# Kernel optimization log

Measured on AMD Instinct MI355X. Metric: run time of the kernel, lower is better.

Reference implementation:

```python
import jax, jax.numpy as jnp
import numpy as np

N = 100000
E = 3200000
IN_CH = 512
H1 = 16


def setup_inputs() -> dict:
    key = jax.random.key(0)
    ks = jax.random.split(key, 9)
    x = jax.random.normal(ks[0], (N, IN_CH), dtype=jnp.float32)
    edge_index = jax.random.randint(ks[1], (2, E), 0, N, dtype=jnp.int64)
    # GCNConv params: weight [in, out], bias [out]
    def glorot(k, fan_in, fan_out):
        lim = (6.0 / (fan_in + fan_out)) ** 0.5
        return jax.random.uniform(k, (fan_in, fan_out), jnp.float32, -lim, lim)
    W1 = glorot(ks[2], IN_CH, H1)
    b1 = jnp.zeros((H1,), jnp.float32)
    W2 = glorot(ks[3], H1, H1)
    b2 = jnp.zeros((H1,), jnp.float32)
    W3 = glorot(ks[4], H1, 1)
    b3 = jnp.zeros((1,), jnp.float32)
    return {"x": x, "edge_index": edge_index, "W1": W1, "b1": b1,
            "W2": W2, "b2": b2, "W3": W3, "b3": b3}


def _gcn_conv(x, W, b, src, dst, deg_isqrt):
    # GCNConv: h = X W; out = D^-1/2 (A + I) D^-1/2 h + b
    h = x @ W  # [N, out]
    norm = deg_isqrt[src] * deg_isqrt[dst]  # [E]
    msg = h[src] * norm[:, None]  # gather + scale
    agg = jax.ops.segment_sum(msg, dst, num_segments=N)  # scatter-add
    agg = agg + h * (deg_isqrt * deg_isqrt)[:, None]  # self-loop term
    return agg + b


def reference(x, edge_index, W1, b1, W2, b2, W3, b3):
    src, dst = edge_index[0], edge_index[1]
    # degree of A + I, counted on destination nodes (symmetric norm)
    deg = jax.ops.segment_sum(jnp.ones((E,), jnp.float32), dst, num_segments=N) + 1.0
    deg_isqrt = jax.lax.rsqrt(deg)
    h = _gcn_conv(x, W1, b1, src, dst, deg_isqrt)
    h = jax.nn.relu(h)  # dropout is identity at eval
    h = _gcn_conv(h, W2, b2, src, dst, deg_isqrt)
    h = jax.nn.relu(h)
    out = _gcn_conv(h, W3, b3, src, dst, deg_isqrt)
    return out
```

## Files before the change

### kernel.cpp

```cpp
#include <hip/hip_runtime.h>
#include <hip/hip_bf16.h>

static constexpr int N_NODES = 100000;
static constexpr int N_EDGES = 3200000;
static constexpr int IN_CH = 512;
static constexpr int H = 16;
static constexpr int TB = 256;

static constexpr int BN = 256;
static constexpr int NB = (N_NODES + BN - 1) / BN;
static constexpr int CAP = 8960;
static constexpr int CAP2 = CAP + 3 * BN;
static constexpr int CHUNK = 8192;
static constexpr int GRID_SC = (N_EDGES + CHUNK - 1) / CHUNK;
static constexpr int NBLK64 = (N_NODES + 63) / 64;

__global__ void k_init(int* __restrict__ gcur) {
  int b = blockIdx.x * blockDim.x + threadIdx.x;
  if (b < NB) gcur[b] = b * CAP;
}

__global__ void k_cscatter(const int* __restrict__ ei, int* __restrict__ gcur,
                           int* __restrict__ ebuf) {
  __shared__ int cnt[NB];
  __shared__ int gofs[NB];
  int t = threadIdx.x;
  int c0 = blockIdx.x * CHUNK;
  int c1 = min(c0 + CHUNK, N_EDGES);
  for (int b = t; b < NB; b += TB) cnt[b] = 0;
  __syncthreads();
  for (int j = c0 + t; j < c1; j += TB) atomicAdd(&cnt[ei[N_EDGES + j] >> 8], 1);
  __syncthreads();
  for (int b = t; b < NB; b += TB)
    if (cnt[b] > 0) gofs[b] = atomicAdd(&gcur[b], cnt[b]);
  __syncthreads();
  for (int j = c0 + t; j < c1; j += TB) {
    int s = ei[j];
    int d = ei[N_EDGES + j];
    int slot = atomicAdd(&gofs[d >> 8], 1);
    ebuf[slot] = ((d & 255) << 17) | s;
  }
}

__global__ void k_bsort(const int* __restrict__ gcur, const int* __restrict__ ebuf,
                        int* __restrict__ ebuf2, int* __restrict__ nrs,
                        int* __restrict__ nend, float* __restrict__ disq) {
  __shared__ int cnt[BN];
  __shared__ int pre[BN];
  __shared__ int cur[BN];
  int b = blockIdx.x, t = threadIdx.x;
  cnt[t] = 0;
  __syncthreads();
  int beg = b * CAP, end = gcur[b];
  for (int j = beg + t; j < end; j += TB) atomicAdd(&cnt[ebuf[j] >> 17], 1);
  __syncthreads();
  int myc = cnt[t];
  int ac = (myc + 3) & ~3;
  pre[t] = ac;
  __syncthreads();
  for (int off = 1; off < TB; off <<= 1) {
    int v = (t >= off) ? pre[t - off] : 0;
    __syncthreads();
    pre[t] += v;
    __syncthreads();
  }
  int start = b * CAP2 + ((t == 0) ? 0 : pre[t - 1]);
  cur[t] = start;
  int node = b * BN + t;
  if (node < N_NODES) {
    nrs[node] = start;
    nend[node] = start + ac;
    disq[node] = 1.0f / sqrtf((float)myc + 1.0f);
    for (int j = start + myc; j < start + ac; j++) ebuf2[j] = N_NODES;
  }
  __syncthreads();
  for (int j = beg + t; j < end; j += TB) {
    int p = ebuf[j];
    int slot = atomicAdd(&cur[p >> 17], 1);
    ebuf2[slot] = p & 0x1FFFF;
  }
}

__global__ void k_gemm1(const float* __restrict__ x, const float* __restrict__ W,
                        const float* __restrict__ disq,
                        float* __restrict__ hA, float* __restrict__ hB,
                        float* __restrict__ hs3) {
  int r = blockIdx.x * blockDim.x + threadIdx.x;
  if (r > N_NODES) return;
  float4* oa = (float4*)(hA + (size_t)r * 16);
  if (r == N_NODES) {
    float4 z = make_float4(0.f, 0.f, 0.f, 0.f);
    float4* ob = (float4*)(hB + (size_t)r * 16);
#pragma unroll
    for (int i = 0; i < 4; i++) { oa[i] = z; ob[i] = z; }
    hs3[r] = 0.f;
    return;
  }
  const float4* xr = (const float4*)(x + (size_t)r * IN_CH);
  float acc[H];
#pragma unroll
  for (int c = 0; c < H; c++) acc[c] = 0.f;
  for (int k4 = 0; k4 < IN_CH / 4; k4++) {
    float4 xv = xr[k4];
    const float* wr = W + k4 * 4 * H;
    float xs[4] = {xv.x, xv.y, xv.z, xv.w};
#pragma unroll
    for (int j = 0; j < 4; j++) {
#pragma unroll
      for (int c = 0; c < H; c++) acc[c] = fmaf(xs[j], wr[j * H + c], acc[c]);
    }
  }
  float dn = disq[r];
  oa[0] = make_float4(acc[0] * dn, acc[1] * dn, acc[2] * dn, acc[3] * dn);
  oa[1] = make_float4(acc[4] * dn, acc[5] * dn, acc[6] * dn, acc[7] * dn);
  oa[2] = make_float4(acc[8] * dn, acc[9] * dn, acc[10] * dn, acc[11] * dn);
  oa[3] = make_float4(acc[12] * dn, acc[13] * dn, acc[14] * dn, acc[15] * dn);
}

__global__ void k_gath_mid(const int* __restrict__ nrs, const int* __restrict__ nend,
                           const int* __restrict__ ebuf2, const float* __restrict__ disq,
                           const float* __restrict__ hin, const float* __restrict__ W2,
                           const float* __restrict__ bias, float* __restrict__ hout) {
  __shared__ float agg[64 * 20];
  __shared__ float w[256];
  int b = blockIdx.x, t = threadIdx.x;
  w[t] = W2[t];
  int nl = t >> 2, q = t & 3;
  int node = b * 64 + nl;
  const float4* hin4 = (const float4*)hin;
  if (node < N_NODES) {
    int beg = nrs[node], endp = nend[node];
    float4 acc = make_float4(0.f, 0.f, 0.f, 0.f);
    for (int j = beg; j < endp; j += 4) {
      int4 s = *(const int4*)(ebuf2 + j);
      float4 a0 = hin4[s.x * 4 + q];
      float4 a1 = hin4[s.y * 4 + q];
      float4 a2 = hin4[s.z * 4 + q];
      float4 a3 = hin4[s.w * 4 + q];
      acc.x += (a0.x + a1.x) + (a2.x + a3.x);
      acc.y += (a0.y + a1.y) + (a2.y + a3.y);
      acc.z += (a0.z + a1.z) + (a2.z + a3.z);
      acc.w += (a0.w + a1.w) + (a2.w + a3.w);
    }
    float4 sf = hin4[node * 4 + q];
    float dn = disq[node];
    float4 bi = *(const float4*)(bias + q * 4);
    float4 r;
    r.x = fmaf(acc.x + sf.x, dn, bi.x);
    r.y = fmaf(acc.y + sf.y, dn, bi.y);
    r.z = fmaf(acc.z + sf.z, dn, bi.z);
    r.w = fmaf(acc.w + sf.w, dn, bi.w);
    *(float4*)(agg + nl * 20 + q * 4) = r;
  }
  __syncthreads();
  if (node < N_NODES) {
    float o0 = 0.f, o1 = 0.f, o2 = 0.f, o3 = 0.f;
#pragma unroll
    for (int c4 = 0; c4 < 4; c4++) {
      float4 av = *(const float4*)(agg + nl * 20 + c4 * 4);
      float vs[4] = {av.x, av.y, av.z, av.w};
#pragma unroll
      for (int i2 = 0; i2 < 4; i2++) {
        float v = fmaxf(vs[i2], 0.f);
        const float* wr = w + (c4 * 4 + i2) * 16 + q * 4;
        o0 = fmaf(v, wr[0], o0);
        o1 = fmaf(v, wr[1], o1);
        o2 = fmaf(v, wr[2], o2);
        o3 = fmaf(v, wr[3], o3);
      }
    }
    float dn = disq[node];
    *(float4*)(hout + (size_t)node * 16 + q * 4) =
        make_float4(o0 * dn, o1 * dn, o2 * dn, o3 * dn);
  }
}

__global__ void k_gath_last(const int* __restrict__ nrs, const int* __restrict__ nend,
                            const int* __restrict__ ebuf2, const float* __restrict__ disq,
                            const float* __restrict__ hin, const float* __restrict__ W3,
                            const float* __restrict__ bias, float* __restrict__ hs3) {
  int b = blockIdx.x, t = threadIdx.x;
  int nl = t >> 2, q = t & 3;
  int node = b * 64 + nl;
  if (node >= N_NODES) return;
  const float4* hin4 = (const float4*)hin;
  int beg = nrs[node], endp = nend[node];
  float4 acc = make_float4(0.f, 0.f, 0.f, 0.f);
  for (int j = beg; j < endp; j += 4) {
    int4 s = *(const int4*)(ebuf2 + j);
    float4 a0 = hin4[s.x * 4 + q];
    float4 a1 = hin4[s.y * 4 + q];
    float4 a2 = hin4[s.z * 4 + q];
    float4 a3 = hin4[s.w * 4 + q];
    acc.x += (a0.x + a1.x) + (a2.x + a3.x);
    acc.y += (a0.y + a1.y) + (a2.y + a3.y);
    acc.z += (a0.z + a1.z) + (a2.z + a3.z);
    acc.w += (a0.w + a1.w) + (a2.w + a3.w);
  }
  float4 sf = hin4[node * 4 + q];
  float dn = disq[node];
  float4 bi = *(const float4*)(bias + q * 4);
  float4 w3 = *(const float4*)(W3 + q * 4);
  float v0 = fmaxf(fmaf(acc.x + sf.x, dn, bi.x), 0.f);
  float v1 = fmaxf(fmaf(acc.y + sf.y, dn, bi.y), 0.f);
  float v2 = fmaxf(fmaf(acc.z + sf.z, dn, bi.z), 0.f);
  float v3 = fmaxf(fmaf(acc.w + sf.w, dn, bi.w), 0.f);
  float o = v0 * w3.x;
  o = fmaf(v1, w3.y, o);
  o = fmaf(v2, w3.z, o);
  o = fmaf(v3, w3.w, o);
  o += __shfl_xor(o, 1);
  o += __shfl_xor(o, 2);
  if (q == 0) hs3[node] = o * dn;
}

__global__ void k_gath1(const int* __restrict__ nrs, const int* __restrict__ nend,
                        const int* __restrict__ ebuf2, const float* __restrict__ disq,
                        const float* __restrict__ hs3, const float* __restrict__ bias,
                        float* __restrict__ out) {
  int b = blockIdx.x, t = threadIdx.x;
  int nl = t >> 2, lane = t & 3;
  int node = b * 64 + nl;
  if (node >= N_NODES) return;
  int beg = nrs[node], endp = nend[node];
  float acc = 0.f;
  for (int j = beg + 4 * lane; j < endp; j += 16) {
    int4 s = *(const int4*)(ebuf2 + j);
    acc += (hs3[s.x] + hs3[s.y]) + (hs3[s.z] + hs3[s.w]);
  }
  acc += __shfl_xor(acc, 1);
  acc += __shfl_xor(acc, 2);
  if (lane == 0) out[node] = fmaf(acc + hs3[node], disq[node], bias[0]);
}

extern "C" void kernel_launch(void* const* d_in, const int* in_sizes, int n_in,
                              void* d_out, int out_size, void* d_ws, size_t ws_size,
                              hipStream_t stream) {
  const float* x = (const float*)d_in[0];
  const int* ei = (const int*)d_in[1];
  const float* W1 = (const float*)d_in[2];
  const float* b1 = (const float*)d_in[3];
  const float* W2 = (const float*)d_in[4];
  const float* b2 = (const float*)d_in[5];
  const float* W3 = (const float*)d_in[6];
  const float* b3 = (const float*)d_in[7];
  float* out = (float*)d_out;

  int* ebuf = (int*)d_ws;
  int* ebuf2 = ebuf + (size_t)NB * CAP;
  int* gcur = ebuf2 + (size_t)NB * CAP2;
  int* nrs = gcur + NB;
  int* nend = nrs + N_NODES;
  int pad = (4 - ((NB + 2 * N_NODES) & 3)) & 3;
  float* disq = (float*)(nend + N_NODES + pad);
  float* hA = disq + N_NODES;
  float* hB = hA + (size_t)(N_NODES + 1) * 16;
  float* hs3 = hB + (size_t)(N_NODES + 1) * 16;

  k_init<<<(NB + 63) / 64, 64, 0, stream>>>(gcur);
  k_cscatter<<<GRID_SC, TB, 0, stream>>>(ei, gcur, ebuf);
  k_bsort<<<NB, TB, 0, stream>>>(gcur, ebuf, ebuf2, nrs, nend, disq);

  k_gemm1<<<(N_NODES + 64) / 64, 64, 0, stream>>>(x, W1, disq, hA, hB, hs3);
  k_gath_mid<<<NBLK64, TB, 0, stream>>>(nrs, nend, ebuf2, disq, hA, W2, b1, hB);
  k_gath_last<<<NBLK64, TB, 0, stream>>>(nrs, nend, ebuf2, disq, hB, W3, b2, hs3);
  k_gath1<<<NBLK64, TB, 0, stream>>>(nrs, nend, ebuf2, disq, hs3, b3, out);
}
```

Measured before the change: 557.2 us.

## Split 16-wide feature tables into two 8-wide halves for cache-resident gathers

The 16-channel node feature tables are split into two 8-channel halves of about 3.2MB each, and each half is gathered in its own pass. The goal is to keep each gather table resident in L2 or the infinity cache. The dense W2/W3 transforms move out of the gather kernels into separate per-node kernels, and edge-index loads and aggregate stores become nontemporal. This doubles the number of passes over the edge list, since ebuf2 is now read twice per layer, and adds extra round trips through global memory for the aggregates.

```diff
diff --git a/kernel.cpp b/kernel.cpp
--- a/kernel.cpp
+++ b/kernel.cpp
@@ -1,5 +1,4 @@
 #include <hip/hip_runtime.h>
-#include <hip/hip_bf16.h>
 
 static constexpr int N_NODES = 100000;
 static constexpr int N_EDGES = 3200000;
@@ -14,6 +13,10 @@
 static constexpr int CHUNK = 8192;
 static constexpr int GRID_SC = (N_EDGES + CHUNK - 1) / CHUNK;
 static constexpr int NBLK64 = (N_NODES + 63) / 64;
+static constexpr int NBLK128 = (N_NODES + 127) / 128;
+
+typedef int vi4 __attribute__((ext_vector_type(4)));
+typedef float vf4 __attribute__((ext_vector_type(4)));
 
 __global__ void k_init(int* __restrict__ gcur) {
   int b = blockIdx.x * blockDim.x + threadIdx.x;
@@ -83,17 +86,14 @@
 
 __global__ void k_gemm1(const float* __restrict__ x, const float* __restrict__ W,
                         const float* __restrict__ disq,
-                        float* __restrict__ hA, float* __restrict__ hB,
-                        float* __restrict__ hs3) {
+                        float* __restrict__ tlo, float* __restrict__ thi) {
   int r = blockIdx.x * blockDim.x + threadIdx.x;
   if (r > N_NODES) return;
-  float4* oa = (float4*)(hA + (size_t)r * 16);
+  float4* olo = (float4*)(tlo + (size_t)r * 8);
+  float4* ohi = (float4*)(thi + (size_t)r * 8);
   if (r == N_NODES) {
     float4 z = make_float4(0.f, 0.f, 0.f, 0.f);
-    float4* ob = (float4*)(hB + (size_t)r * 16);
-#pragma unroll
-    for (int i = 0; i < 4; i++) { oa[i] = z; ob[i] = z; }
-    hs3[r] = 0.f;
+    olo[0] = z; olo[1] = z; ohi[0] = z; ohi[1] = z;
     return;
   }
   const float4* xr = (const float4*)(x + (size_t)r * IN_CH);
@@ -111,107 +111,119 @@
     }
   }
   float dn = disq[r];
-  oa[0] = make_float4(acc[0] * dn, acc[1] * dn, acc[2] * dn, acc[3] * dn);
-  oa[1] = make_float4(acc[4] * dn, acc[5] * dn, acc[6] * dn, acc[7] * dn);
-  oa[2] = make_float4(acc[8] * dn, acc[9] * dn, acc[10] * dn, acc[11] * dn);
-  oa[3] = make_float4(acc[12] * dn, acc[13] * dn, acc[14] * dn, acc[15] * dn);
-}
-
-__global__ void k_gath_mid(const int* __restrict__ nrs, const int* __restrict__ nend,
-                           const int* __restrict__ ebuf2, const float* __restrict__ disq,
-                           const float* __restrict__ hin, const float* __restrict__ W2,
-                           const float* __restrict__ bias, float* __restrict__ hout) {
-  __shared__ float agg[64 * 20];
-  __shared__ float w[256];
+  olo[0] = make_float4(acc[0] * dn, acc[1] * dn, acc[2] * dn, acc[3] * dn);
+  olo[1] = make_float4(acc[4] * dn, acc[5] * dn, acc[6] * dn, acc[7] * dn);
+  ohi[0] = make_float4(acc[8] * dn, acc[9] * dn, acc[10] * dn, acc[11] * dn);
+  ohi[1] = make_float4(acc[12] * dn, acc[13] * dn, acc[14] * dn, acc[15] * dn);
+}
+
+__global__ void k_gath8(const int* __restrict__ nrs, const int* __restrict__ nend,
+                        const int* __restrict__ ebuf2, const float* __restrict__ disq,
+                        const float* __restrict__ tbl, float* __restrict__ agg) {
   int b = blockIdx.x, t = threadIdx.x;
-  w[t] = W2[t];
-  int nl = t >> 2, q = t & 3;
-  int node = b * 64 + nl;
-  const float4* hin4 = (const float4*)hin;
-  if (node < N_NODES) {
-    int beg = nrs[node], endp = nend[node];
-    float4 acc = make_float4(0.f, 0.f, 0.f, 0.f);
-    for (int j = beg; j < endp; j += 4) {
-      int4 s = *(const int4*)(ebuf2 + j);
-      float4 a0 = hin4[s.x * 4 + q];
-      float4 a1 = hin4[s.y * 4 + q];
-      float4 a2 = hin4[s.z * 4 + q];
-      float4 a3 = hin4[s.w * 4 + q];
-      acc.x += (a0.x + a1.x) + (a2.x + a3.x);
-      acc.y += (a0.y + a1.y) + (a2.y + a3.y);
-      acc.z += (a0.z + a1.z) + (a2.z + a3.z);
-      acc.w += (a0.w + a1.w) + (a2.w + a3.w);
-    }
-    float4 sf = hin4[node * 4 + q];
-    float dn = disq[node];
-    float4 bi = *(const float4*)(bias + q * 4);
-    float4 r;
-    r.x = fmaf(acc.x + sf.x, dn, bi.x);
-    r.y = fmaf(acc.y + sf.y, dn, bi.y);
-    r.z = fmaf(acc.z + sf.z, dn, bi.z);
-    r.w = fmaf(acc.w + sf.w, dn, bi.w);
-    *(float4*)(agg + nl * 20 + q * 4) = r;
-  }
-  __syncthreads();
-  if (node < N_NODES) {
-    float o0 = 0.f, o1 = 0.f, o2 = 0.f, o3 = 0.f;
-#pragma unroll
-    for (int c4 = 0; c4 < 4; c4++) {
-      float4 av = *(const float4*)(agg + nl * 20 + c4 * 4);
-      float vs[4] = {av.x, av.y, av.z, av.w};
-#pragma unroll
-      for (int i2 = 0; i2 < 4; i2++) {
-        float v = fmaxf(vs[i2], 0.f);
-        const float* wr = w + (c4 * 4 + i2) * 16 + q * 4;
-        o0 = fmaf(v, wr[0], o0);
-        o1 = fmaf(v, wr[1], o1);
-        o2 = fmaf(v, wr[2], o2);
-        o3 = fmaf(v, wr[3], o3);
-      }
-    }
-    float dn = disq[node];
-    *(float4*)(hout + (size_t)node * 16 + q * 4) =
-        make_float4(o0 * dn, o1 * dn, o2 * dn, o3 * dn);
-  }
-}
-
-__global__ void k_gath_last(const int* __restrict__ nrs, const int* __restrict__ nend,
-                            const int* __restrict__ ebuf2, const float* __restrict__ disq,
-                            const float* __restrict__ hin, const float* __restrict__ W3,
-                            const float* __restrict__ bias, float* __restrict__ hs3) {
-  int b = blockIdx.x, t = threadIdx.x;
-  int nl = t >> 2, q = t & 3;
-  int node = b * 64 + nl;
+  int nl = t >> 1, q = t & 1;
+  int node = b * 128 + nl;
   if (node >= N_NODES) return;
-  const float4* hin4 = (const float4*)hin;
+  const float4* t4 = (const float4*)tbl;
   int beg = nrs[node], endp = nend[node];
   float4 acc = make_float4(0.f, 0.f, 0.f, 0.f);
   for (int j = beg; j < endp; j += 4) {
-    int4 s = *(const int4*)(ebuf2 + j);
-    float4 a0 = hin4[s.x * 4 + q];
-    float4 a1 = hin4[s.y * 4 + q];
-    float4 a2 = hin4[s.z * 4 + q];
-    float4 a3 = hin4[s.w * 4 + q];
+    vi4 s = __builtin_nontemporal_load((const vi4*)(ebuf2 + j));
+    float4 a0 = t4[s.x * 2 + q];
+    float4 a1 = t4[s.y * 2 + q];
+    float4 a2 = t4[s.z * 2 + q];
+    float4 a3 = t4[s.w * 2 + q];
     acc.x += (a0.x + a1.x) + (a2.x + a3.x);
     acc.y += (a0.y + a1.y) + (a2.y + a3.y);
     acc.z += (a0.z + a1.z) + (a2.z + a3.z);
     acc.w += (a0.w + a1.w) + (a2.w + a3.w);
   }
-  float4 sf = hin4[node * 4 + q];
+  float4 sf = t4[node * 2 + q];
   float dn = disq[node];
-  float4 bi = *(const float4*)(bias + q * 4);
-  float4 w3 = *(const float4*)(W3 + q * 4);
-  float v0 = fmaxf(fmaf(acc.x + sf.x, dn, bi.x), 0.f);
-  float v1 = fmaxf(fmaf(acc.y + sf.y, dn, bi.y), 0.f);
-  float v2 = fmaxf(fmaf(acc.z + sf.z, dn, bi.z), 0.f);
-  float v3 = fmaxf(fmaf(acc.w + sf.w, dn, bi.w), 0.f);
-  float o = v0 * w3.x;
-  o = fmaf(v1, w3.y, o);
-  o = fmaf(v2, w3.z, o);
-  o = fmaf(v3, w3.w, o);
-  o += __shfl_xor(o, 1);
-  o += __shfl_xor(o, 2);
-  if (q == 0) hs3[node] = o * dn;
+  vf4 r;
+  r.x = (acc.x + sf.x) * dn;
+  r.y = (acc.y + sf.y) * dn;
+  r.z = (acc.z + sf.z) * dn;
+  r.w = (acc.w + sf.w) * dn;
+  __builtin_nontemporal_store(r, (vf4*)(agg + (size_t)node * 8 + q * 4));
+}
+
+__global__ void k_mid(const float* __restrict__ aggLo, const float* __restrict__ aggHi,
+                      const float* __restrict__ W2, const float* __restrict__ bias,
+                      const float* __restrict__ disq,
+                      float* __restrict__ tlo, float* __restrict__ thi) {
+  __shared__ float w[256];
+  int t = threadIdx.x;
+  w[t] = W2[t];
+  __syncthreads();
+  int r = blockIdx.x * 256 + t;
+  if (r > N_NODES) return;
+  float4* olo = (float4*)(tlo + (size_t)r * 8);
+  float4* ohi = (float4*)(thi + (size_t)r * 8);
+  if (r == N_NODES) {
+    float4 z = make_float4(0.f, 0.f, 0.f, 0.f);
+    olo[0] = z; olo[1] = z; ohi[0] = z; ohi[1] = z;
+    return;
+  }
+  float v[16];
+  float4 a;
+  a = *(const float4*)(aggLo + (size_t)r * 8);
+  v[0] = a.x; v[1] = a.y; v[2] = a.z; v[3] = a.w;
+  a = *(const float4*)(aggLo + (size_t)r * 8 + 4);
+  v[4] = a.x; v[5] = a.y; v[6] = a.z; v[7] = a.w;
+  a = *(const float4*)(aggHi + (size_t)r * 8);
+  v[8] = a.x; v[9] = a.y; v[10] = a.z; v[11] = a.w;
+  a = *(const float4*)(aggHi + (size_t)r * 8 + 4);
+  v[12] = a.x; v[13] = a.y; v[14] = a.z; v[15] = a.w;
+#pragma unroll
+  for (int i = 0; i < 16; i++) v[i] = fmaxf(v[i] + bias[i], 0.f);
+  float4 o[4];
+#pragma unroll
+  for (int c4 = 0; c4 < 4; c4++) o[c4] = make_float4(0.f, 0.f, 0.f, 0.f);
+#pragma unroll
+  for (int i = 0; i < 16; i++) {
+    float vi = v[i];
+#pragma unroll
+    for (int c4 = 0; c4 < 4; c4++) {
+      float4 wv = *(const float4*)(w + i * 16 + c4 * 4);
+      o[c4].x = fmaf(vi, wv.x, o[c4].x);
+      o[c4].y = fmaf(vi, wv.y, o[c4].y);
+      o[c4].z = fmaf(vi, wv.z, o[c4].z);
+      o[c4].w = fmaf(vi, wv.w, o[c4].w);
+    }
+  }
+  float dn = disq[r];
+#pragma unroll
+  for (int c4 = 0; c4 < 4; c4++) {
+    o[c4].x *= dn; o[c4].y *= dn; o[c4].z *= dn; o[c4].w *= dn;
+  }
+  olo[0] = o[0]; olo[1] = o[1]; ohi[0] = o[2]; ohi[1] = o[3];
+}
+
+__global__ void k_last(const float* __restrict__ aggLo, const float* __restrict__ aggHi,
+                       const float* __restrict__ W3, const float* __restrict__ bias,
+                       const float* __restrict__ disq, float* __restrict__ hs3) {
+  __shared__ float w3[16];
+  int t = threadIdx.x;
+  if (t < 16) w3[t] = W3[t];
+  __syncthreads();
+  int r = blockIdx.x * 256 + t;
+  if (r > N_NODES) return;
+  if (r == N_NODES) { hs3[r] = 0.f; return; }
+  float v[16];
+  float4 a;
+  a = *(const float4*)(aggLo + (size_t)r * 8);
+  v[0] = a.x; v[1] = a.y; v[2] = a.z; v[3] = a.w;
+  a = *(const float4*)(aggLo + (size_t)r * 8 + 4);
+  v[4] = a.x; v[5] = a.y; v[6] = a.z; v[7] = a.w;
+  a = *(const float4*)(aggHi + (size_t)r * 8);
+  v[8] = a.x; v[9] = a.y; v[10] = a.z; v[11] = a.w;
+  a = *(const float4*)(aggHi + (size_t)r * 8 + 4);
+  v[12] = a.x; v[13] = a.y; v[14] = a.z; v[15] = a.w;
+  float o = 0.f;
+#pragma unroll
+  for (int i = 0; i < 16; i++) o = fmaf(fmaxf(v[i] + bias[i], 0.f), w3[i], o);
+  hs3[r] = o * disq[r];
 }
 
 __global__ void k_gath1(const int* __restrict__ nrs, const int* __restrict__ nend,
@@ -225,7 +237,7 @@
   int beg = nrs[node], endp = nend[node];
   float acc = 0.f;
   for (int j = beg + 4 * lane; j < endp; j += 16) {
-    int4 s = *(const int4*)(ebuf2 + j);
+    vi4 s = __builtin_nontemporal_load((const vi4*)(ebuf2 + j));
     acc += (hs3[s.x] + hs3[s.y]) + (hs3[s.z] + hs3[s.w]);
   }
   acc += __shfl_xor(acc, 1);
@@ -253,16 +265,24 @@
   int* nend = nrs + N_NODES;
   int pad = (4 - ((NB + 2 * N_NODES) & 3)) & 3;
   float* disq = (float*)(nend + N_NODES + pad);
-  float* hA = disq + N_NODES;
-  float* hB = hA + (size_t)(N_NODES + 1) * 16;
-  float* hs3 = hB + (size_t)(N_NODES + 1) * 16;
+  float* tloA = disq + N_NODES;
+  float* thiA = tloA + (size_t)(N_NODES + 1) * 8;
+  float* tloB = thiA + (size_t)(N_NODES + 1) * 8;
+  float* thiB = tloB + (size_t)(N_NODES + 1) * 8;
+  float* aggLo = thiB + (size_t)(N_NODES + 1) * 8;
+  float* aggHi = aggLo + (size_t)N_NODES * 8;
+  float* hs3 = aggHi + (size_t)N_NODES * 8;
 
   k_init<<<(NB + 63) / 64, 64, 0, stream>>>(gcur);
   k_cscatter<<<GRID_SC, TB, 0, stream>>>(ei, gcur, ebuf);
   k_bsort<<<NB, TB, 0, stream>>>(gcur, ebuf, ebuf2, nrs, nend, disq);
 
-  k_gemm1<<<(N_NODES + 64) / 64, 64, 0, stream>>>(x, W1, disq, hA, hB, hs3);
-  k_gath_mid<<<NBLK64, TB, 0, stream>>>(nrs, nend, ebuf2, disq, hA, W2, b1, hB);
-  k_gath_last<<<NBLK64, TB, 0, stream>>>(nrs, nend, ebuf2, disq, hB, W3, b2, hs3);
+  k_gemm1<<<(N_NODES + 64) / 64, 64, 0, stream>>>(x, W1, disq, tloA, thiA);
+  k_gath8<<<NBLK128, TB, 0, stream>>>(nrs, nend, ebuf2, disq, tloA, aggLo);
+  k_gath8<<<NBLK128, TB, 0, stream>>>(nrs, nend, ebuf2, disq, thiA, aggHi);
+  k_mid<<<(N_NODES + 256) / 256, 256, 0, stream>>>(aggLo, aggHi, W2, b1, disq, tloB, thiB);
+  k_gath8<<<NBLK128, TB, 0, stream>>>(nrs, nend, ebuf2, disq, tloB, aggLo);
+  k_gath8<<<NBLK128, TB, 0, stream>>>(nrs, nend, ebuf2, disq, thiB, aggHi);
+  k_last<<<(N_NODES + 256) / 256, 256, 0, stream>>>(aggLo, aggHi, W3, b2, disq, hs3);
   k_gath1<<<NBLK64, TB, 0, stream>>>(nrs, nend, ebuf2, disq, hs3, b3, out);
 }
```

New measurement: 617.0 us. 1.11x slower.

## Fuse all GCN stages into one persistent cooperative kernel with grid syncs

Applied to the files above, without the earlier changes.

Replaces the seven separate launches (bucket init, scatter, bucket sort, layer-1 GEMM, and the three gather layers) with a single cooperative kernel that loops over work with grid-stride loops and separates phases with grid-wide barriers. The intent is to remove per-launch overhead and inter-kernel gaps. In exchange, the grid is capped by occupancy, so phases run with fewer resident blocks, and register pressure from the merged code may reduce occupancy; grid.sync adds its own barrier cost.

```diff
diff --git a/kernel.cpp b/kernel.cpp
--- a/kernel.cpp
+++ b/kernel.cpp
@@ -1,5 +1,7 @@
 #include <hip/hip_runtime.h>
-#include <hip/hip_bf16.h>
+#include <hip/hip_cooperative_groups.h>
+
+namespace cg = cooperative_groups;
 
 static constexpr int N_NODES = 100000;
 static constexpr int N_EDGES = 3200000;
@@ -15,222 +17,228 @@
 static constexpr int GRID_SC = (N_EDGES + CHUNK - 1) / CHUNK;
 static constexpr int NBLK64 = (N_NODES + 63) / 64;
 
-__global__ void k_init(int* __restrict__ gcur) {
-  int b = blockIdx.x * blockDim.x + threadIdx.x;
-  if (b < NB) gcur[b] = b * CAP;
-}
-
-__global__ void k_cscatter(const int* __restrict__ ei, int* __restrict__ gcur,
-                           int* __restrict__ ebuf) {
-  __shared__ int cnt[NB];
-  __shared__ int gofs[NB];
-  int t = threadIdx.x;
-  int c0 = blockIdx.x * CHUNK;
-  int c1 = min(c0 + CHUNK, N_EDGES);
-  for (int b = t; b < NB; b += TB) cnt[b] = 0;
-  __syncthreads();
-  for (int j = c0 + t; j < c1; j += TB) atomicAdd(&cnt[ei[N_EDGES + j] >> 8], 1);
-  __syncthreads();
-  for (int b = t; b < NB; b += TB)
-    if (cnt[b] > 0) gofs[b] = atomicAdd(&gcur[b], cnt[b]);
-  __syncthreads();
-  for (int j = c0 + t; j < c1; j += TB) {
-    int s = ei[j];
-    int d = ei[N_EDGES + j];
-    int slot = atomicAdd(&gofs[d >> 8], 1);
-    ebuf[slot] = ((d & 255) << 17) | s;
-  }
-}
-
-__global__ void k_bsort(const int* __restrict__ gcur, const int* __restrict__ ebuf,
-                        int* __restrict__ ebuf2, int* __restrict__ nrs,
-                        int* __restrict__ nend, float* __restrict__ disq) {
-  __shared__ int cnt[BN];
-  __shared__ int pre[BN];
-  __shared__ int cur[BN];
-  int b = blockIdx.x, t = threadIdx.x;
-  cnt[t] = 0;
-  __syncthreads();
-  int beg = b * CAP, end = gcur[b];
-  for (int j = beg + t; j < end; j += TB) atomicAdd(&cnt[ebuf[j] >> 17], 1);
-  __syncthreads();
-  int myc = cnt[t];
-  int ac = (myc + 3) & ~3;
-  pre[t] = ac;
-  __syncthreads();
-  for (int off = 1; off < TB; off <<= 1) {
-    int v = (t >= off) ? pre[t - off] : 0;
-    __syncthreads();
-    pre[t] += v;
-    __syncthreads();
-  }
-  int start = b * CAP2 + ((t == 0) ? 0 : pre[t - 1]);
-  cur[t] = start;
-  int node = b * BN + t;
-  if (node < N_NODES) {
-    nrs[node] = start;
-    nend[node] = start + ac;
-    disq[node] = 1.0f / sqrtf((float)myc + 1.0f);
-    for (int j = start + myc; j < start + ac; j++) ebuf2[j] = N_NODES;
-  }
-  __syncthreads();
-  for (int j = beg + t; j < end; j += TB) {
-    int p = ebuf[j];
-    int slot = atomicAdd(&cur[p >> 17], 1);
-    ebuf2[slot] = p & 0x1FFFF;
-  }
-}
-
-__global__ void k_gemm1(const float* __restrict__ x, const float* __restrict__ W,
-                        const float* __restrict__ disq,
-                        float* __restrict__ hA, float* __restrict__ hB,
-                        float* __restrict__ hs3) {
-  int r = blockIdx.x * blockDim.x + threadIdx.x;
-  if (r > N_NODES) return;
-  float4* oa = (float4*)(hA + (size_t)r * 16);
-  if (r == N_NODES) {
-    float4 z = make_float4(0.f, 0.f, 0.f, 0.f);
-    float4* ob = (float4*)(hB + (size_t)r * 16);
-#pragma unroll
-    for (int i = 0; i < 4; i++) { oa[i] = z; ob[i] = z; }
-    hs3[r] = 0.f;
-    return;
-  }
-  const float4* xr = (const float4*)(x + (size_t)r * IN_CH);
-  float acc[H];
-#pragma unroll
-  for (int c = 0; c < H; c++) acc[c] = 0.f;
-  for (int k4 = 0; k4 < IN_CH / 4; k4++) {
-    float4 xv = xr[k4];
-    const float* wr = W + k4 * 4 * H;
-    float xs[4] = {xv.x, xv.y, xv.z, xv.w};
-#pragma unroll
-    for (int j = 0; j < 4; j++) {
-#pragma unroll
-      for (int c = 0; c < H; c++) acc[c] = fmaf(xs[j], wr[j * H + c], acc[c]);
-    }
-  }
-  float dn = disq[r];
-  oa[0] = make_float4(acc[0] * dn, acc[1] * dn, acc[2] * dn, acc[3] * dn);
-  oa[1] = make_float4(acc[4] * dn, acc[5] * dn, acc[6] * dn, acc[7] * dn);
-  oa[2] = make_float4(acc[8] * dn, acc[9] * dn, acc[10] * dn, acc[11] * dn);
-  oa[3] = make_float4(acc[12] * dn, acc[13] * dn, acc[14] * dn, acc[15] * dn);
-}
-
-__global__ void k_gath_mid(const int* __restrict__ nrs, const int* __restrict__ nend,
-                           const int* __restrict__ ebuf2, const float* __restrict__ disq,
-                           const float* __restrict__ hin, const float* __restrict__ W2,
-                           const float* __restrict__ bias, float* __restrict__ hout) {
+__global__ __launch_bounds__(TB, 4) void k_fused(
+    const float* __restrict__ x, const int* __restrict__ ei,
+    const float* __restrict__ W1, const float* __restrict__ b1,
+    const float* __restrict__ W2, const float* __restrict__ b2,
+    const float* __restrict__ W3, const float* __restrict__ b3,
+    float* __restrict__ out,
+    int* __restrict__ ebuf, int* __restrict__ ebuf2, int* __restrict__ gcur,
+    int* __restrict__ nrs, int* __restrict__ nend, float* __restrict__ disq,
+    float* __restrict__ hA, float* __restrict__ hB, float* __restrict__ hs3) {
+  cg::grid_group grid = cg::this_grid();
+  __shared__ int scnt[NB];
+  __shared__ int sofs[NB];
+  __shared__ int cur2[BN];
   __shared__ float agg[64 * 20];
   __shared__ float w[256];
-  int b = blockIdx.x, t = threadIdx.x;
+  int t = threadIdx.x;
+  int wg = blockIdx.x, nwg = gridDim.x;
+  int gid = wg * TB + t;
+  int nthr = nwg * TB;
+
+  for (int b = gid; b < NB; b += nthr) gcur[b] = b * CAP;
+  grid.sync();
+
+  for (int c = wg; c < GRID_SC; c += nwg) {
+    int c0 = c * CHUNK, c1 = min(c0 + CHUNK, N_EDGES);
+    for (int b = t; b < NB; b += TB) scnt[b] = 0;
+    __syncthreads();
+    for (int j = c0 + t; j < c1; j += TB) atomicAdd(&scnt[ei[N_EDGES + j] >> 8], 1);
+    __syncthreads();
+    for (int b = t; b < NB; b += TB)
+      if (scnt[b] > 0) sofs[b] = atomicAdd(&gcur[b], scnt[b]);
+    __syncthreads();
+    for (int j = c0 + t; j < c1; j += TB) {
+      int s = ei[j];
+      int d = ei[N_EDGES + j];
+      int slot = atomicAdd(&sofs[d >> 8], 1);
+      ebuf[slot] = ((d & 255) << 17) | s;
+    }
+    __syncthreads();
+  }
+  grid.sync();
+
+  for (int b = wg; b < NB; b += nwg) {
+    scnt[t] = 0;
+    __syncthreads();
+    int beg = b * CAP, end = gcur[b];
+    for (int j = beg + t; j < end; j += TB) atomicAdd(&scnt[ebuf[j] >> 17], 1);
+    __syncthreads();
+    int myc = scnt[t];
+    int ac = (myc + 3) & ~3;
+    sofs[t] = ac;
+    __syncthreads();
+    for (int off = 1; off < TB; off <<= 1) {
+      int v = (t >= off) ? sofs[t - off] : 0;
+      __syncthreads();
+      sofs[t] += v;
+      __syncthreads();
+    }
+    int start = b * CAP2 + ((t == 0) ? 0 : sofs[t - 1]);
+    cur2[t] = start;
+    int node = b * BN + t;
+    if (node < N_NODES) {
+      nrs[node] = start;
+      nend[node] = start + ac;
+      disq[node] = 1.0f / sqrtf((float)myc + 1.0f);
+      for (int j = start + myc; j < start + ac; j++) ebuf2[j] = N_NODES;
+    }
+    __syncthreads();
+    for (int j = beg + t; j < end; j += TB) {
+      int p = ebuf[j];
+      int slot = atomicAdd(&cur2[p >> 17], 1);
+      ebuf2[slot] = p & 0x1FFFF;
+    }
+    __syncthreads();
+  }
+  grid.sync();
+
+  for (int r = gid; r <= N_NODES; r += nthr) {
+    float4* oa = (float4*)(hA + (size_t)r * 16);
+    if (r == N_NODES) {
+      float4 z = make_float4(0.f, 0.f, 0.f, 0.f);
+      float4* ob = (float4*)(hB + (size_t)r * 16);
+#pragma unroll
+      for (int i = 0; i < 4; i++) { oa[i] = z; ob[i] = z; }
+      hs3[r] = 0.f;
+      continue;
+    }
+    const float4* xr = (const float4*)(x + (size_t)r * IN_CH);
+    float acc[H];
+#pragma unroll
+    for (int c = 0; c < H; c++) acc[c] = 0.f;
+    for (int k4 = 0; k4 < IN_CH / 4; k4++) {
+      float4 xv = xr[k4];
+      const float* wr = W1 + k4 * 4 * H;
+      float xs[4] = {xv.x, xv.y, xv.z, xv.w};
+#pragma unroll
+      for (int j = 0; j < 4; j++) {
+#pragma unroll
+        for (int c = 0; c < H; c++) acc[c] = fmaf(xs[j], wr[j * H + c], acc[c]);
+      }
+    }
+    float dn = disq[r];
+    oa[0] = make_float4(acc[0] * dn, acc[1] * dn, acc[2] * dn, acc[3] * dn);
+    oa[1] = make_float4(acc[4] * dn, acc[5] * dn, acc[6] * dn, acc[7] * dn);
+    oa[2] = make_float4(acc[8] * dn, acc[9] * dn, acc[10] * dn, acc[11] * dn);
+    oa[3] = make_float4(acc[12] * dn, acc[13] * dn, acc[14] * dn, acc[15] * dn);
+  }
+  grid.sync();
+
   w[t] = W2[t];
-  int nl = t >> 2, q = t & 3;
-  int node = b * 64 + nl;
-  const float4* hin4 = (const float4*)hin;
-  if (node < N_NODES) {
-    int beg = nrs[node], endp = nend[node];
-    float4 acc = make_float4(0.f, 0.f, 0.f, 0.f);
-    for (int j = beg; j < endp; j += 4) {
-      int4 s = *(const int4*)(ebuf2 + j);
-      float4 a0 = hin4[s.x * 4 + q];
-      float4 a1 = hin4[s.y * 4 + q];
-      float4 a2 = hin4[s.z * 4 + q];
-      float4 a3 = hin4[s.w * 4 + q];
-      acc.x += (a0.x + a1.x) + (a2.x + a3.x);
-      acc.y += (a0.y + a1.y) + (a2.y + a3.y);
-      acc.z += (a0.z + a1.z) + (a2.z + a3.z);
-      acc.w += (a0.w + a1.w) + (a2.w + a3.w);
-    }
-    float4 sf = hin4[node * 4 + q];
-    float dn = disq[node];
-    float4 bi = *(const float4*)(bias + q * 4);
-    float4 r;
-    r.x = fmaf(acc.x + sf.x, dn, bi.x);
-    r.y = fmaf(acc.y + sf.y, dn, bi.y);
-    r.z = fmaf(acc.z + sf.z, dn, bi.z);
-    r.w = fmaf(acc.w + sf.w, dn, bi.w);
-    *(float4*)(agg + nl * 20 + q * 4) = r;
-  }
-  __syncthreads();
-  if (node < N_NODES) {
-    float o0 = 0.f, o1 = 0.f, o2 = 0.f, o3 = 0.f;
-#pragma unroll
-    for (int c4 = 0; c4 < 4; c4++) {
-      float4 av = *(const float4*)(agg + nl * 20 + c4 * 4);
-      float vs[4] = {av.x, av.y, av.z, av.w};
-#pragma unroll
-      for (int i2 = 0; i2 < 4; i2++) {
-        float v = fmaxf(vs[i2], 0.f);
-        const float* wr = w + (c4 * 4 + i2) * 16 + q * 4;
-        o0 = fmaf(v, wr[0], o0);
-        o1 = fmaf(v, wr[1], o1);
-        o2 = fmaf(v, wr[2], o2);
-        o3 = fmaf(v, wr[3], o3);
-      }
-    }
-    float dn = disq[node];
-    *(float4*)(hout + (size_t)node * 16 + q * 4) =
-        make_float4(o0 * dn, o1 * dn, o2 * dn, o3 * dn);
-  }
-}
-
-__global__ void k_gath_last(const int* __restrict__ nrs, const int* __restrict__ nend,
-                            const int* __restrict__ ebuf2, const float* __restrict__ disq,
-                            const float* __restrict__ hin, const float* __restrict__ W3,
-                            const float* __restrict__ bias, float* __restrict__ hs3) {
-  int b = blockIdx.x, t = threadIdx.x;
-  int nl = t >> 2, q = t & 3;
-  int node = b * 64 + nl;
-  if (node >= N_NODES) return;
-  const float4* hin4 = (const float4*)hin;
-  int beg = nrs[node], endp = nend[node];
-  float4 acc = make_float4(0.f, 0.f, 0.f, 0.f);
-  for (int j = beg; j < endp; j += 4) {
-    int4 s = *(const int4*)(ebuf2 + j);
-    float4 a0 = hin4[s.x * 4 + q];
-    float4 a1 = hin4[s.y * 4 + q];
-    float4 a2 = hin4[s.z * 4 + q];
-    float4 a3 = hin4[s.w * 4 + q];
-    acc.x += (a0.x + a1.x) + (a2.x + a3.x);
-    acc.y += (a0.y + a1.y) + (a2.y + a3.y);
-    acc.z += (a0.z + a1.z) + (a2.z + a3.z);
-    acc.w += (a0.w + a1.w) + (a2.w + a3.w);
-  }
-  float4 sf = hin4[node * 4 + q];
-  float dn = disq[node];
-  float4 bi = *(const float4*)(bias + q * 4);
-  float4 w3 = *(const float4*)(W3 + q * 4);
-  float v0 = fmaxf(fmaf(acc.x + sf.x, dn, bi.x), 0.f);
-  float v1 = fmaxf(fmaf(acc.y + sf.y, dn, bi.y), 0.f);
-  float v2 = fmaxf(fmaf(acc.z + sf.z, dn, bi.z), 0.f);
-  float v3 = fmaxf(fmaf(acc.w + sf.w, dn, bi.w), 0.f);
-  float o = v0 * w3.x;
-  o = fmaf(v1, w3.y, o);
-  o = fmaf(v2, w3.z, o);
-  o = fmaf(v3, w3.w, o);
-  o += __shfl_xor(o, 1);
-  o += __shfl_xor(o, 2);
-  if (q == 0) hs3[node] = o * dn;
-}
-
-__global__ void k_gath1(const int* __restrict__ nrs, const int* __restrict__ nend,
-                        const int* __restrict__ ebuf2, const float* __restrict__ disq,
-                        const float* __restrict__ hs3, const float* __restrict__ bias,
-                        float* __restrict__ out) {
-  int b = blockIdx.x, t = threadIdx.x;
-  int nl = t >> 2, lane = t & 3;
-  int node = b * 64 + nl;
-  if (node >= N_NODES) return;
-  int beg = nrs[node], endp = nend[node];
-  float acc = 0.f;
-  for (int j = beg + 4 * lane; j < endp; j += 16) {
-    int4 s = *(const int4*)(ebuf2 + j);
-    acc += (hs3[s.x] + hs3[s.y]) + (hs3[s.z] + hs3[s.w]);
-  }
-  acc += __shfl_xor(acc, 1);
-  acc += __shfl_xor(acc, 2);
-  if (lane == 0) out[node] = fmaf(acc + hs3[node], disq[node], bias[0]);
+  {
+    int nl = t >> 2, q = t & 3;
+    const float4* h4 = (const float4*)hA;
+    for (int blk = wg; blk < NBLK64; blk += nwg) {
+      int node = blk * 64 + nl;
+      if (node < N_NODES) {
+        int beg = nrs[node], endp = nend[node];
+        float4 acc = make_float4(0.f, 0.f, 0.f, 0.f);
+        for (int j = beg; j < endp; j += 4) {
+          int4 s = *(const int4*)(ebuf2 + j);
+          float4 a0 = h4[s.x * 4 + q];
+          float4 a1 = h4[s.y * 4 + q];
+          float4 a2 = h4[s.z * 4 + q];
+          float4 a3 = h4[s.w * 4 + q];
+          acc.x += (a0.x + a1.x) + (a2.x + a3.x);
+          acc.y += (a0.y + a1.y) + (a2.y + a3.y);
+          acc.z += (a0.z + a1.z) + (a2.z + a3.z);
+          acc.w += (a0.w + a1.w) + (a2.w + a3.w);
+        }
+        float4 sf = h4[node * 4 + q];
+        float dn = disq[node];
+        float4 bi = *(const float4*)(b1 + q * 4);
+        float4 r;
+        r.x = fmaf(acc.x + sf.x, dn, bi.x);
+        r.y = fmaf(acc.y + sf.y, dn, bi.y);
+        r.z = fmaf(acc.z + sf.z, dn, bi.z);
+        r.w = fmaf(acc.w + sf.w, dn, bi.w);
+        *(float4*)(agg + nl * 20 + q * 4) = r;
+      }
+      __syncthreads();
+      if (node < N_NODES) {
+        float o0 = 0.f, o1 = 0.f, o2 = 0.f, o3 = 0.f;
+#pragma unroll
+        for (int c4 = 0; c4 < 4; c4++) {
+          float4 av = *(const float4*)(agg + nl * 20 + c4 * 4);
+          float vs[4] = {av.x, av.y, av.z, av.w};
+#pragma unroll
+          for (int i2 = 0; i2 < 4; i2++) {
+            float v = fmaxf(vs[i2], 0.f);
+            const float* wr = w + (c4 * 4 + i2) * 16 + q * 4;
+            o0 = fmaf(v, wr[0], o0);
+            o1 = fmaf(v, wr[1], o1);
+            o2 = fmaf(v, wr[2], o2);
+            o3 = fmaf(v, wr[3], o3);
+          }
+        }
+        float dn = disq[node];
+        *(float4*)(hB + (size_t)node * 16 + q * 4) =
+            make_float4(o0 * dn, o1 * dn, o2 * dn, o3 * dn);
+      }
+      __syncthreads();
+    }
+  }
+  grid.sync();
+
+  {
+    int nl = t >> 2, q = t & 3;
+    const float4* h4 = (const float4*)hB;
+    float4 w3v = *(const float4*)(W3 + q * 4);
+    float4 bi = *(const float4*)(b2 + q * 4);
+    for (int blk = wg; blk < NBLK64; blk += nwg) {
+      int node = blk * 64 + nl;
+      if (node < N_NODES) {
+        int beg = nrs[node], endp = nend[node];
+        float4 acc = make_float4(0.f, 0.f, 0.f, 0.f);
+        for (int j = beg; j < endp; j += 4) {
+          int4 s = *(const int4*)(ebuf2 + j);
+          float4 a0 = h4[s.x * 4 + q];
+          float4 a1 = h4[s.y * 4 + q];
+          float4 a2 = h4[s.z * 4 + q];
+          float4 a3 = h4[s.w * 4 + q];
+          acc.x += (a0.x + a1.x) + (a2.x + a3.x);
+          acc.y += (a0.y + a1.y) + (a2.y + a3.y);
+          acc.z += (a0.z + a1.z) + (a2.z + a3.z);
+          acc.w += (a0.w + a1.w) + (a2.w + a3.w);
+        }
+        float4 sf = h4[node * 4 + q];
+        float dn = disq[node];
+        float v0 = fmaxf(fmaf(acc.x + sf.x, dn, bi.x), 0.f);
+        float v1 = fmaxf(fmaf(acc.y + sf.y, dn, bi.y), 0.f);
+        float v2 = fmaxf(fmaf(acc.z + sf.z, dn, bi.z), 0.f);
+        float v3 = fmaxf(fmaf(acc.w + sf.w, dn, bi.w), 0.f);
+        float o = v0 * w3v.x;
+        o = fmaf(v1, w3v.y, o);
+        o = fmaf(v2, w3v.z, o);
+        o = fmaf(v3, w3v.w, o);
+        o += __shfl_xor(o, 1);
+        o += __shfl_xor(o, 2);
+        if (q == 0) hs3[node] = o * dn;
+      }
+    }
+  }
+  grid.sync();
+
+  {
+    int nl = t >> 2, lane = t & 3;
+    float b3v = b3[0];
+    for (int blk = wg; blk < NBLK64; blk += nwg) {
+      int node = blk * 64 + nl;
+      if (node < N_NODES) {
+        int beg = nrs[node], endp = nend[node];
+        float acc = 0.f;
+        for (int j = beg + 4 * lane; j < endp; j += 16) {
+          int4 s = *(const int4*)(ebuf2 + j);
+          acc += (hs3[s.x] + hs3[s.y]) + (hs3[s.z] + hs3[s.w]);
+        }
+        acc += __shfl_xor(acc, 1);
+        acc += __shfl_xor(acc, 2);
+        if (lane == 0) out[node] = fmaf(acc + hs3[node], disq[node], b3v);
+      }
+    }
+  }
 }
 
 extern "C" void kernel_launch(void* const* d_in, const int* in_sizes, int n_in,
@@ -257,12 +265,18 @@
   float* hB = hA + (size_t)(N_NODES + 1) * 16;
   float* hs3 = hB + (size_t)(N_NODES + 1) * 16;
 
-  k_init<<<(NB + 63) / 64, 64, 0, stream>>>(gcur);
-  k_cscatter<<<GRID_SC, TB, 0, stream>>>(ei, gcur, ebuf);
-  k_bsort<<<NB, TB, 0, stream>>>(gcur, ebuf, ebuf2, nrs, nend, disq);
-
-  k_gemm1<<<(N_NODES + 64) / 64, 64, 0, stream>>>(x, W1, disq, hA, hB, hs3);
-  k_gath_mid<<<NBLK64, TB, 0, stream>>>(nrs, nend, ebuf2, disq, hA, W2, b1, hB);
-  k_gath_last<<<NBLK64, TB, 0, stream>>>(nrs, nend, ebuf2, disq, hB, W3, b2, hs3);
-  k_gath1<<<NBLK64, TB, 0, stream>>>(nrs, nend, ebuf2, disq, hs3, b3, out);
+  static int grid = 0;
+  if (grid == 0) {
+    int nb = 0;
+    (void)hipOccupancyMaxActiveBlocksPerMultiprocessor(&nb, k_fused, TB, 0);
+    if (nb < 1) nb = 1;
+    int cap = nb * 256;
+    grid = cap < 782 ? cap : 782;
+  }
+
+  void* args[] = {(void*)&x,  (void*)&ei,  (void*)&W1, (void*)&b1, (void*)&W2,
+                  (void*)&b2, (void*)&W3,  (void*)&b3, (void*)&out, (void*)&ebuf,
+                  (void*)&ebuf2, (void*)&gcur, (void*)&nrs, (void*)&nend,
+                  (void*)&disq, (void*)&hA, (void*)&hB, (void*)&hs3};
+  hipLaunchCooperativeKernel((void*)k_fused, dim3(grid), dim3(TB), args, 0, stream);
 }
```

After: 1.069 ms. 91.9% more time.
